# Kernel optimization log

Measured on AMD Instinct MI355X. Metric: run time of the kernel, lower is better.

The kernel has to match this reference:

```python
import jax, jax.numpy as jnp
import numpy as np

B, D, H, W, K = 32, 64, 64, 64, 512  # batch, embed_dim (channels), latent HxW, codebook size
BETA = 0.2


def setup_inputs() -> dict:
    key = jax.random.key(0)
    k1, k2 = jax.random.split(key)
    features = jax.random.normal(k1, (B, D, H, W), dtype=jnp.float32)
    emb_weight = jax.random.normal(k2, (K, D), dtype=jnp.float32)
    return {"features": features, "emb_weight": emb_weight}


def reference(features, emb_weight):
    b, d, h, w = features.shape
    # NCHW -> (B, HW, D) channels-last flatten (torch permute(0,2,3,1).view)
    quant_in = features.transpose(0, 2, 3, 1).reshape(b, h * w, d)
    # squared euclidean distances (argmin-equivalent to torch.cdist)
    x2 = jnp.sum(quant_in * quant_in, axis=-1, keepdims=True)          # (B, HW, 1)
    e2 = jnp.sum(emb_weight * emb_weight, axis=-1)                     # (K,)
    dist2 = x2 + e2[None, None, :] - 2.0 * jnp.einsum('bnd,kd->bnk', quant_in, emb_weight)
    min_index = jnp.argmin(dist2, axis=-1)                             # (B, HW)
    quant_out = emb_weight[min_index]                                  # gather, (B, HW, D)
    # commitment + beta * codebook loss (means over all elements)
    commitment_loss = jnp.mean((jax.lax.stop_gradient(quant_out) - quant_in) ** 2)
    codebook_loss = jnp.mean((quant_out - jax.lax.stop_gradient(quant_in)) ** 2)
    quantize_loss = commitment_loss + BETA * codebook_loss
    # straight-through estimator
    st = quant_in + jax.lax.stop_gradient(quant_out - quant_in)
    st = st.reshape(b, h, w, d).transpose(0, 3, 1, 2)                  # back to NCHW
    return st, quantize_loss
```

## Files before the change

### kernel.cpp

```cpp
#include <hip/hip_runtime.h>
#include <hip/hip_bf16.h>

#define BB 32
#define DD 64
#define HWHW 4096
#define NPOS 131072
#define NELEM (NPOS * DD)
#define KK 512
#define LOSS_SCALE (1.2f / 8388608.f)
#define DELTA 2.0f
#define QCAP 4096
#define PT 2
#define NTHR 1024
#define POSB 512
#define NBLK (NPOS / POSB)

typedef __attribute__((ext_vector_type(8))) short short8v;
typedef __attribute__((ext_vector_type(4))) float float4v;

__device__ inline unsigned short f2bf(float f) {
    unsigned u = __float_as_uint(f);
    unsigned r = u + 0x7FFFu + ((u >> 16) & 1u);
    return (unsigned short)(r >> 16);
}
__device__ inline float bf2f(unsigned short s) {
    return __uint_as_float(((unsigned)s) << 16);
}
__device__ inline unsigned f2o(float f) {
    unsigned u = __float_as_uint(f);
    return ((int)u < 0) ? ~u : (u | 0x80000000u);
}

__global__ __launch_bounds__(256) void vq_prep(const float* __restrict__ emb,
                                               unsigned short* __restrict__ ebf,
                                               float* __restrict__ ne2h) {
    const int t = blockIdx.x * 256 + threadIdx.x;
    const int row = t >> 4, c = t & 15;
    const float4 v = *(const float4*)(emb + row * DD + c * 4);
    unsigned u0 = (unsigned)f2bf(v.x) | ((unsigned)f2bf(v.y) << 16);
    unsigned u1 = (unsigned)f2bf(v.z) | ((unsigned)f2bf(v.w) << 16);
    *(uint2*)(ebf + row * DD + c * 4) = make_uint2(u0, u1);
    float p = v.x * v.x + v.y * v.y + v.z * v.z + v.w * v.w;
    p += __shfl_xor(p, 1, 64); p += __shfl_xor(p, 2, 64);
    p += __shfl_xor(p, 4, 64); p += __shfl_xor(p, 8, 64);
    if (c == 0) ne2h[row] = -0.5f * p;
}

__global__ __launch_bounds__(NTHR) void vq_main(
        const float* __restrict__ feat,
        const float* __restrict__ emb,
        const unsigned short* __restrict__ ebf,
        const float* __restrict__ ne2h,
        float* __restrict__ out,
        float* __restrict__ loss) {

    __shared__ uint4 ebf_lds[4096];
    __shared__ float ne2_lds[KK];
    __shared__ unsigned long long sbest[POSB];
    __shared__ unsigned qbuf[QCAP];
    __shared__ unsigned qcnt;
    __shared__ float wsum[NTHR / 64];

    const int tid = threadIdx.x;
    const int wid = tid >> 6, lane = tid & 63;
    const int l15 = lane & 15, lg = lane >> 4;

    {
        const uint4* src = (const uint4*)ebf;
#pragma unroll
        for (int i = 0; i < 4; ++i) {
            const int idx = tid * 4 + i;
            const int row = idx >> 3, c = idx & 7;
            ebf_lds[row * 8 + (c ^ (row & 7))] = src[idx];
        }
    }
    if (tid < KK) ne2_lds[tid] = ne2h[tid];
    if (tid < POSB) sbest[tid] = 0ull;
    if (tid == 0) qcnt = 0u;

    const int pbase = blockIdx.x * POSB;
    const int b     = pbase >> 12;
    const int hwb   = pbase & 4095;
    const float* featB = feat + (size_t)b * DD * HWHW;
    float*       outB  = out  + (size_t)b * DD * HWHW;
    const int wbase = wid * (PT * 16);

    float xv[PT][2][8];
#pragma unroll
    for (int pt = 0; pt < PT; ++pt) {
        const int hw = hwb + wbase + pt * 16 + l15;
#pragma unroll
        for (int h = 0; h < 2; ++h)
#pragma unroll
            for (int j = 0; j < 8; ++j)
                xv[pt][h][j] = featB[(size_t)(h * 32 + lg * 8 + j) * HWHW + hw];
    }
    short8v bx[PT][2];
#pragma unroll
    for (int pt = 0; pt < PT; ++pt)
#pragma unroll
        for (int h = 0; h < 2; ++h) {
            short8v s;
#pragma unroll
            for (int j = 0; j < 8; ++j) s[j] = (short)f2bf(xv[pt][h][j]);
            bx[pt][h] = s;
        }

    __syncthreads();

    const int swz = l15 & 7;
    const uint4* a0p = &ebf_lds[l15 * 8 + (lg ^ swz)];
    const uint4* a1p = &ebf_lds[l15 * 8 + ((lg | 4) ^ swz)];

    float M[PT];
#pragma unroll
    for (int pt = 0; pt < PT; ++pt) M[pt] = -3.0e38f;

    short8v a0n = *(const short8v*)a0p;
    short8v a1n = *(const short8v*)a1p;
    float4v ne2n = *(const float4v*)&ne2_lds[lg * 4];

    for (int ct = 0; ct < 32; ++ct) {
        const short8v a0c = a0n, a1c = a1n;
        const float4v ne2c = ne2n;
        if (ct < 31) {
            a0n = *(const short8v*)(a0p + (ct + 1) * 128);
            a1n = *(const short8v*)(a1p + (ct + 1) * 128);
            ne2n = *(const float4v*)&ne2_lds[(ct + 1) * 16 + lg * 4];
        }
        float4v acc[PT];
#pragma unroll
        for (int pt = 0; pt < PT; ++pt)
            acc[pt] = __builtin_amdgcn_mfma_f32_16x16x32_bf16(a0c, bx[pt][0], ne2c, 0, 0, 0);
#pragma unroll
        for (int pt = 0; pt < PT; ++pt)
            acc[pt] = __builtin_amdgcn_mfma_f32_16x16x32_bf16(a1c, bx[pt][1], acc[pt], 0, 0, 0);
#pragma unroll
        for (int pt = 0; pt < PT; ++pt) {
            const float m01 = fmaxf(acc[pt][0], acc[pt][1]);
            const float m23 = fmaxf(acc[pt][2], acc[pt][3]);
            M[pt] = fmaxf(M[pt], fmaxf(m01, m23));
        }
    }

    float thr[PT];
#pragma unroll
    for (int pt = 0; pt < PT; ++pt) {
        float m = M[pt];
        m = fmaxf(m, __shfl_xor(m, 16, 64));
        m = fmaxf(m, __shfl_xor(m, 32, 64));
        thr[pt] = m - DELTA;
    }

    a0n = *(const short8v*)a0p;
    a1n = *(const short8v*)a1p;
    ne2n = *(const float4v*)&ne2_lds[lg * 4];

    for (int ct = 0; ct < 32; ++ct) {
        const short8v a0c = a0n, a1c = a1n;
        const float4v ne2c = ne2n;
        if (ct < 31) {
            a0n = *(const short8v*)(a0p + (ct + 1) * 128);
            a1n = *(const short8v*)(a1p + (ct + 1) * 128);
            ne2n = *(const float4v*)&ne2_lds[(ct + 1) * 16 + lg * 4];
        }
        float4v acc[PT];
#pragma unroll
        for (int pt = 0; pt < PT; ++pt)
            acc[pt] = __builtin_amdgcn_mfma_f32_16x16x32_bf16(a0c, bx[pt][0], ne2c, 0, 0, 0);
#pragma unroll
        for (int pt = 0; pt < PT; ++pt)
            acc[pt] = __builtin_amdgcn_mfma_f32_16x16x32_bf16(a1c, bx[pt][1], acc[pt], 0, 0, 0);
#pragma unroll
        for (int pt = 0; pt < PT; ++pt) {
            const float m01 = fmaxf(acc[pt][0], acc[pt][1]);
            const float m23 = fmaxf(acc[pt][2], acc[pt][3]);
            const float mx  = fmaxf(m01, m23);
            if (__any(mx >= thr[pt])) {
#pragma unroll
                for (int r = 0; r < 4; ++r) {
                    if (acc[pt][r] >= thr[pt]) {
                        const unsigned idx  = atomicAdd(&qcnt, 1u);
                        const unsigned code = (unsigned)(ct * 16 + lg * 4 + r);
                        const unsigned pos  = (unsigned)(wbase + pt * 16 + l15);
                        if (idx < QCAP) qbuf[idx] = (pos << 9) | code;
                    }
                }
            }
        }
    }

    __syncthreads();

    const unsigned qn  = qcnt;
    const bool     ovf = (qn > (unsigned)QCAP);
    const unsigned n   = ovf ? (unsigned)(POSB * KK) : qn;
    for (unsigned i = tid; i < n; i += NTHR) {
        unsigned p, k;
        if (ovf) { p = i >> 9; k = i & 511u; }
        else     { const unsigned e = qbuf[i]; p = e >> 9; k = e & 511u; }
        const float4* er4 = (const float4*)(emb + k * DD);
        const float*  fp  = featB + hwb + p;
        float a0 = 0.f, a1 = 0.f;
#pragma unroll 4
        for (int dq = 0; dq < 16; ++dq) {
            const float4 e4 = er4[dq];
            a0 = fmaf(fp[(size_t)(4 * dq    ) * HWHW], e4.x, a0);
            a1 = fmaf(fp[(size_t)(4 * dq + 1) * HWHW], e4.y, a1);
            a0 = fmaf(fp[(size_t)(4 * dq + 2) * HWHW], e4.z, a0);
            a1 = fmaf(fp[(size_t)(4 * dq + 3) * HWHW], e4.w, a1);
        }
        const float sc = (a0 + a1) + ne2h[k];
        const unsigned long long key =
            ((unsigned long long)f2o(sc) << 32) | (unsigned long long)(511u - k);
        atomicMax(&sbest[p], key);
    }

    __syncthreads();

    float lsum = 0.f;
#pragma unroll
    for (int pt = 0; pt < PT; ++pt) {
        const int pl = wbase + pt * 16 + l15;
        const int hw = hwb + pl;
        const unsigned long long key = sbest[pl];
        const unsigned k = 511u - (unsigned)key;
        const float* er = emb + k * DD;
#pragma unroll
        for (int h = 0; h < 2; ++h) {
            const short8v xs = bx[pt][h];
#pragma unroll
            for (int jj = 0; jj < 2; ++jj) {
                const float4v ev = *(const float4v*)(er + h * 32 + lg * 8 + jj * 4);
#pragma unroll
                for (int c = 0; c < 4; ++c) {
                    const int j = jj * 4 + c;
                    const int d = h * 32 + lg * 8 + j;
                    const float q = ev[c];
                    outB[(size_t)d * HWHW + hw] = q;
                    const float diff = q - bf2f((unsigned short)xs[j]);
                    lsum = fmaf(diff, diff, lsum);
                }
            }
        }
    }

#pragma unroll
    for (int off = 32; off > 0; off >>= 1) lsum += __shfl_down(lsum, off, 64);
    if (lane == 0) wsum[wid] = lsum;
    __syncthreads();
    if (tid == 0) {
        float s = 0.f;
#pragma unroll
        for (int w = 0; w < NTHR / 64; ++w) s += wsum[w];
        atomicAdd(loss, s * LOSS_SCALE);
    }
}

extern "C" void kernel_launch(void* const* d_in, const int* in_sizes, int n_in,
                              void* d_out, int out_size, void* d_ws, size_t ws_size,
                              hipStream_t stream) {
    const float* feat = (const float*)d_in[0];
    const float* emb  = (const float*)d_in[1];
    float* out  = (float*)d_out;
    float* loss = out + NELEM;

    unsigned short* ebf  = (unsigned short*)d_ws;
    float*          ne2h = (float*)((char*)d_ws + 64 * 1024);

    hipMemsetAsync(loss, 0, sizeof(float), stream);
    vq_prep<<<dim3(32), dim3(256), 0, stream>>>(emb, ebf, ne2h);
    vq_main<<<dim3(NBLK), dim3(NTHR), 0, stream>>>(feat, emb, ebf, ne2h, out, loss);
}
```

Before: 135.0 us.

## Fuse max pass and candidate collection into single pass with running threshold

```diff
diff --git a/kernel.cpp b/kernel.cpp
--- a/kernel.cpp
+++ b/kernel.cpp
@@ -112,7 +112,7 @@
     const uint4* a0p = &ebf_lds[l15 * 8 + (lg ^ swz)];
     const uint4* a1p = &ebf_lds[l15 * 8 + ((lg | 4) ^ swz)];
 
-    float M[PT];
+    float M[PT], thr[PT];
 #pragma unroll
     for (int pt = 0; pt < PT; ++pt) M[pt] = -3.0e38f;
 
@@ -120,14 +120,12 @@
     short8v a1n = *(const short8v*)a1p;
     float4v ne2n = *(const float4v*)&ne2_lds[lg * 4];
 
-    for (int ct = 0; ct < 32; ++ct) {
+    for (int ct = 0; ct < 4; ++ct) {
         const short8v a0c = a0n, a1c = a1n;
         const float4v ne2c = ne2n;
-        if (ct < 31) {
-            a0n = *(const short8v*)(a0p + (ct + 1) * 128);
-            a1n = *(const short8v*)(a1p + (ct + 1) * 128);
-            ne2n = *(const float4v*)&ne2_lds[(ct + 1) * 16 + lg * 4];
-        }
+        a0n = *(const short8v*)(a0p + (ct + 1) * 128);
+        a1n = *(const short8v*)(a1p + (ct + 1) * 128);
+        ne2n = *(const float4v*)&ne2_lds[(ct + 1) * 16 + lg * 4];
         float4v acc[PT];
 #pragma unroll
         for (int pt = 0; pt < PT; ++pt)
@@ -137,33 +135,22 @@
             acc[pt] = __builtin_amdgcn_mfma_f32_16x16x32_bf16(a1c, bx[pt][1], acc[pt], 0, 0, 0);
 #pragma unroll
         for (int pt = 0; pt < PT; ++pt) {
-            const float m01 = fmaxf(acc[pt][0], acc[pt][1]);
-            const float m23 = fmaxf(acc[pt][2], acc[pt][3]);
-            M[pt] = fmaxf(M[pt], fmaxf(m01, m23));
-        }
-    }
-
-    float thr[PT];
+            const float m4 = fmaxf(fmaxf(fmaxf(acc[pt][0], acc[pt][1]), acc[pt][2]), acc[pt][3]);
+            M[pt] = fmaxf(M[pt], m4);
+        }
+    }
 #pragma unroll
     for (int pt = 0; pt < PT; ++pt) {
         float m = M[pt];
         m = fmaxf(m, __shfl_xor(m, 16, 64));
         m = fmaxf(m, __shfl_xor(m, 32, 64));
-        thr[pt] = m - DELTA;
-    }
-
-    a0n = *(const short8v*)a0p;
-    a1n = *(const short8v*)a1p;
-    ne2n = *(const float4v*)&ne2_lds[lg * 4];
-
-    for (int ct = 0; ct < 32; ++ct) {
-        const short8v a0c = a0n, a1c = a1n;
-        const float4v ne2c = ne2n;
-        if (ct < 31) {
-            a0n = *(const short8v*)(a0p + (ct + 1) * 128);
-            a1n = *(const short8v*)(a1p + (ct + 1) * 128);
-            ne2n = *(const float4v*)&ne2_lds[(ct + 1) * 16 + lg * 4];
-        }
+        M[pt] = m; thr[pt] = m - DELTA;
+    }
+
+    for (int ct = 0; ct < 4; ++ct) {
+        const short8v a0c = *(const short8v*)(a0p + ct * 128);
+        const short8v a1c = *(const short8v*)(a1p + ct * 128);
+        const float4v ne2c = *(const float4v*)&ne2_lds[ct * 16 + lg * 4];
         float4v acc[PT];
 #pragma unroll
         for (int pt = 0; pt < PT; ++pt)
@@ -173,10 +160,8 @@
             acc[pt] = __builtin_amdgcn_mfma_f32_16x16x32_bf16(a1c, bx[pt][1], acc[pt], 0, 0, 0);
 #pragma unroll
         for (int pt = 0; pt < PT; ++pt) {
-            const float m01 = fmaxf(acc[pt][0], acc[pt][1]);
-            const float m23 = fmaxf(acc[pt][2], acc[pt][3]);
-            const float mx  = fmaxf(m01, m23);
-            if (__any(mx >= thr[pt])) {
+            const float m4 = fmaxf(fmaxf(fmaxf(acc[pt][0], acc[pt][1]), acc[pt][2]), acc[pt][3]);
+            if (__any(m4 >= thr[pt])) {
 #pragma unroll
                 for (int r = 0; r < 4; ++r) {
                     if (acc[pt][r] >= thr[pt]) {
@@ -186,6 +171,48 @@
                         if (idx < QCAP) qbuf[idx] = (pos << 9) | code;
                     }
                 }
+            }
+        }
+    }
+
+    for (int ct = 4; ct < 32; ++ct) {
+        const short8v a0c = a0n, a1c = a1n;
+        const float4v ne2c = ne2n;
+        if (ct < 31) {
+            a0n = *(const short8v*)(a0p + (ct + 1) * 128);
+            a1n = *(const short8v*)(a1p + (ct + 1) * 128);
+            ne2n = *(const float4v*)&ne2_lds[(ct + 1) * 16 + lg * 4];
+        }
+        float4v acc[PT];
+#pragma unroll
+        for (int pt = 0; pt < PT; ++pt)
+            acc[pt] = __builtin_amdgcn_mfma_f32_16x16x32_bf16(a0c, bx[pt][0], ne2c, 0, 0, 0);
+#pragma unroll
+        for (int pt = 0; pt < PT; ++pt)
+            acc[pt] = __builtin_amdgcn_mfma_f32_16x16x32_bf16(a1c, bx[pt][1], acc[pt], 0, 0, 0);
+#pragma unroll
+        for (int pt = 0; pt < PT; ++pt) {
+            const float m4 = fmaxf(fmaxf(fmaxf(acc[pt][0], acc[pt][1]), acc[pt][2]), acc[pt][3]);
+            M[pt] = fmaxf(M[pt], m4);
+            if (__any(m4 >= thr[pt])) {
+#pragma unroll
+                for (int r = 0; r < 4; ++r) {
+                    if (acc[pt][r] >= thr[pt]) {
+                        const unsigned idx  = atomicAdd(&qcnt, 1u);
+                        const unsigned code = (unsigned)(ct * 16 + lg * 4 + r);
+                        const unsigned pos  = (unsigned)(wbase + pt * 16 + l15);
+                        if (idx < QCAP) qbuf[idx] = (pos << 9) | code;
+                    }
+                }
+            }
+        }
+        if ((ct & 3) == 3) {
+#pragma unroll
+            for (int pt = 0; pt < PT; ++pt) {
+                float m = M[pt];
+                m = fmaxf(m, __shfl_xor(m, 16, 64));
+                m = fmaxf(m, __shfl_xor(m, 32, 64));
+                M[pt] = m; thr[pt] = m - DELTA;
             }
         }
     }
```

After: 178.9 us. 32.4% more time.

## Split codebook across two wave halves, each wave handling four position tiles

Applied to the files above, without the earlier changes.

```diff
diff --git a/kernel.cpp b/kernel.cpp
--- a/kernel.cpp
+++ b/kernel.cpp
@@ -10,7 +10,7 @@
 #define LOSS_SCALE (1.2f / 8388608.f)
 #define DELTA 2.0f
 #define QCAP 4096
-#define PT 2
+#define PT 4
 #define NTHR 1024
 #define POSB 512
 #define NBLK (NPOS / POSB)
@@ -56,6 +56,7 @@
 
     __shared__ uint4 ebf_lds[4096];
     __shared__ float ne2_lds[KK];
+    __shared__ float pmax2[2][POSB];
     __shared__ unsigned long long sbest[POSB];
     __shared__ unsigned qbuf[QCAP];
     __shared__ unsigned qcnt;
@@ -64,6 +65,8 @@
     const int tid = threadIdx.x;
     const int wid = tid >> 6, lane = tid & 63;
     const int l15 = lane & 15, lg = lane >> 4;
+    const int half = wid >> 3;
+    const int wg   = wid & 7;
 
     {
         const uint4* src = (const uint4*)ebf;
@@ -83,34 +86,38 @@
     const int hwb   = pbase & 4095;
     const float* featB = feat + (size_t)b * DD * HWHW;
     float*       outB  = out  + (size_t)b * DD * HWHW;
-    const int wbase = wid * (PT * 16);
-
-    float xv[PT][2][8];
-#pragma unroll
-    for (int pt = 0; pt < PT; ++pt) {
-        const int hw = hwb + wbase + pt * 16 + l15;
-#pragma unroll
-        for (int h = 0; h < 2; ++h)
-#pragma unroll
-            for (int j = 0; j < 8; ++j)
-                xv[pt][h][j] = featB[(size_t)(h * 32 + lg * 8 + j) * HWHW + hw];
-    }
+    const int wbase = wg * (PT * 16);
+    const int kbase = half * 256;
+
     short8v bx[PT][2];
 #pragma unroll
-    for (int pt = 0; pt < PT; ++pt)
-#pragma unroll
-        for (int h = 0; h < 2; ++h) {
-            short8v s;
-#pragma unroll
-            for (int j = 0; j < 8; ++j) s[j] = (short)f2bf(xv[pt][h][j]);
-            bx[pt][h] = s;
-        }
+    for (int pp = 0; pp < 2; ++pp) {
+        float xv[2][2][8];
+#pragma unroll
+        for (int q = 0; q < 2; ++q) {
+            const int hw = hwb + wbase + (pp * 2 + q) * 16 + l15;
+#pragma unroll
+            for (int h = 0; h < 2; ++h)
+#pragma unroll
+                for (int j = 0; j < 8; ++j)
+                    xv[q][h][j] = featB[(size_t)(h * 32 + lg * 8 + j) * HWHW + hw];
+        }
+#pragma unroll
+        for (int q = 0; q < 2; ++q)
+#pragma unroll
+            for (int h = 0; h < 2; ++h) {
+                short8v s;
+#pragma unroll
+                for (int j = 0; j < 8; ++j) s[j] = (short)f2bf(xv[q][h][j]);
+                bx[pp * 2 + q][h] = s;
+            }
+    }
 
     __syncthreads();
 
     const int swz = l15 & 7;
-    const uint4* a0p = &ebf_lds[l15 * 8 + (lg ^ swz)];
-    const uint4* a1p = &ebf_lds[l15 * 8 + ((lg | 4) ^ swz)];
+    const uint4* a0p = &ebf_lds[(kbase + l15) * 8 + (lg ^ swz)];
+    const uint4* a1p = &ebf_lds[(kbase + l15) * 8 + ((lg | 4) ^ swz)];
 
     float M[PT];
 #pragma unroll
@@ -118,15 +125,15 @@
 
     short8v a0n = *(const short8v*)a0p;
     short8v a1n = *(const short8v*)a1p;
-    float4v ne2n = *(const float4v*)&ne2_lds[lg * 4];
-
-    for (int ct = 0; ct < 32; ++ct) {
+    float4v ne2n = *(const float4v*)&ne2_lds[kbase + lg * 4];
+
+    for (int ct = 0; ct < 16; ++ct) {
         const short8v a0c = a0n, a1c = a1n;
         const float4v ne2c = ne2n;
-        if (ct < 31) {
+        if (ct < 15) {
             a0n = *(const short8v*)(a0p + (ct + 1) * 128);
             a1n = *(const short8v*)(a1p + (ct + 1) * 128);
-            ne2n = *(const float4v*)&ne2_lds[(ct + 1) * 16 + lg * 4];
+            ne2n = *(const float4v*)&ne2_lds[kbase + (ct + 1) * 16 + lg * 4];
         }
         float4v acc[PT];
 #pragma unroll
@@ -143,26 +150,33 @@
         }
     }
 
-    float thr[PT];
 #pragma unroll
     for (int pt = 0; pt < PT; ++pt) {
         float m = M[pt];
         m = fmaxf(m, __shfl_xor(m, 16, 64));
         m = fmaxf(m, __shfl_xor(m, 32, 64));
-        thr[pt] = m - DELTA;
+        if (lg == 0) pmax2[half][wbase + pt * 16 + l15] = m;
+    }
+    __syncthreads();
+
+    float thr[PT];
+#pragma unroll
+    for (int pt = 0; pt < PT; ++pt) {
+        const int pos = wbase + pt * 16 + l15;
+        thr[pt] = fmaxf(pmax2[0][pos], pmax2[1][pos]) - DELTA;
     }
 
     a0n = *(const short8v*)a0p;
     a1n = *(const short8v*)a1p;
-    ne2n = *(const float4v*)&ne2_lds[lg * 4];
-
-    for (int ct = 0; ct < 32; ++ct) {
+    ne2n = *(const float4v*)&ne2_lds[kbase + lg * 4];
+
+    for (int ct = 0; ct < 16; ++ct) {
         const short8v a0c = a0n, a1c = a1n;
         const float4v ne2c = ne2n;
-        if (ct < 31) {
+        if (ct < 15) {
             a0n = *(const short8v*)(a0p + (ct + 1) * 128);
             a1n = *(const short8v*)(a1p + (ct + 1) * 128);
-            ne2n = *(const float4v*)&ne2_lds[(ct + 1) * 16 + lg * 4];
+            ne2n = *(const float4v*)&ne2_lds[kbase + (ct + 1) * 16 + lg * 4];
         }
         float4v acc[PT];
 #pragma unroll
@@ -181,7 +195,7 @@
                 for (int r = 0; r < 4; ++r) {
                     if (acc[pt][r] >= thr[pt]) {
                         const unsigned idx  = atomicAdd(&qcnt, 1u);
-                        const unsigned code = (unsigned)(ct * 16 + lg * 4 + r);
+                        const unsigned code = (unsigned)(kbase + ct * 16 + lg * 4 + r);
                         const unsigned pos  = (unsigned)(wbase + pt * 16 + l15);
                         if (idx < QCAP) qbuf[idx] = (pos << 9) | code;
                     }
@@ -210,7 +224,7 @@
             a0 = fmaf(fp[(size_t)(4 * dq + 2) * HWHW], e4.z, a0);
             a1 = fmaf(fp[(size_t)(4 * dq + 3) * HWHW], e4.w, a1);
         }
-        const float sc = (a0 + a1) + ne2h[k];
+        const float sc = (a0 + a1) + ne2_lds[k];
         const unsigned long long key =
             ((unsigned long long)f2o(sc) << 32) | (unsigned long long)(511u - k);
         atomicMax(&sbest[p], key);
@@ -220,7 +234,8 @@
 
     float lsum = 0.f;
 #pragma unroll
-    for (int pt = 0; pt < PT; ++pt) {
+    for (int q = 0; q < 2; ++q) {
+        const int pt = half * 2 + q;
         const int pl = wbase + pt * 16 + l15;
         const int hw = hwb + pl;
         const unsigned long long key = sbest[pl];
@@ -236,9 +251,9 @@
                 for (int c = 0; c < 4; ++c) {
                     const int j = jj * 4 + c;
                     const int d = h * 32 + lg * 8 + j;
-                    const float q = ev[c];
-                    outB[(size_t)d * HWHW + hw] = q;
-                    const float diff = q - bf2f((unsigned short)xs[j]);
+                    const float q2 = ev[c];
+                    outB[(size_t)d * HWHW + hw] = q2;
+                    const float diff = q2 - bf2f((unsigned short)xs[j]);
                     lsum = fmaf(diff, diff, lsum);
                 }
             }
```

Result: slower. 274.3 us (+103.1%).

## Cache per-tile maxima in fp16 registers to skip second-pass MFMA tiles

Applied to the files above, without the earlier changes.

```diff
diff --git a/kernel.cpp b/kernel.cpp
--- a/kernel.cpp
+++ b/kernel.cpp
@@ -1,5 +1,6 @@
 #include <hip/hip_runtime.h>
 #include <hip/hip_bf16.h>
+#include <hip/hip_fp16.h>
 
 #define BB 32
 #define DD 64
@@ -9,6 +10,7 @@
 #define KK 512
 #define LOSS_SCALE (1.2f / 8388608.f)
 #define DELTA 2.0f
+#define MARG 0.0625f
 #define QCAP 4096
 #define PT 2
 #define NTHR 1024
@@ -29,6 +31,11 @@
 __device__ inline unsigned f2o(float f) {
     unsigned u = __float_as_uint(f);
     return ((int)u < 0) ? ~u : (u | 0x80000000u);
+}
+__device__ inline unsigned packh2(float a, float b) {
+    unsigned lo = (unsigned)__half_as_ushort(__float2half(a));
+    unsigned hi = (unsigned)__half_as_ushort(__float2half(b));
+    return lo | (hi << 16);
 }
 
 __global__ __launch_bounds__(256) void vq_prep(const float* __restrict__ emb,
@@ -112,78 +119,78 @@
     const uint4* a0p = &ebf_lds[l15 * 8 + (lg ^ swz)];
     const uint4* a1p = &ebf_lds[l15 * 8 + ((lg | 4) ^ swz)];
 
-    float M[PT];
-#pragma unroll
-    for (int pt = 0; pt < PT; ++pt) M[pt] = -3.0e38f;
-
-    short8v a0n = *(const short8v*)a0p;
-    short8v a1n = *(const short8v*)a1p;
-    float4v ne2n = *(const float4v*)&ne2_lds[lg * 4];
-
+    float M0 = -3.0e38f, M1 = -3.0e38f;
+    unsigned cache_u[32];
+
+#pragma unroll
     for (int ct = 0; ct < 32; ++ct) {
-        const short8v a0c = a0n, a1c = a1n;
-        const float4v ne2c = ne2n;
-        if (ct < 31) {
-            a0n = *(const short8v*)(a0p + (ct + 1) * 128);
-            a1n = *(const short8v*)(a1p + (ct + 1) * 128);
-            ne2n = *(const float4v*)&ne2_lds[(ct + 1) * 16 + lg * 4];
-        }
-        float4v acc[PT];
-#pragma unroll
-        for (int pt = 0; pt < PT; ++pt)
-            acc[pt] = __builtin_amdgcn_mfma_f32_16x16x32_bf16(a0c, bx[pt][0], ne2c, 0, 0, 0);
-#pragma unroll
-        for (int pt = 0; pt < PT; ++pt)
-            acc[pt] = __builtin_amdgcn_mfma_f32_16x16x32_bf16(a1c, bx[pt][1], acc[pt], 0, 0, 0);
-#pragma unroll
-        for (int pt = 0; pt < PT; ++pt) {
-            const float m01 = fmaxf(acc[pt][0], acc[pt][1]);
-            const float m23 = fmaxf(acc[pt][2], acc[pt][3]);
-            M[pt] = fmaxf(M[pt], fmaxf(m01, m23));
-        }
+        const short8v a0c = *(const short8v*)(a0p + ct * 128);
+        const short8v a1c = *(const short8v*)(a1p + ct * 128);
+        const float4v ne2c = *(const float4v*)&ne2_lds[ct * 16 + lg * 4];
+        float4v acc0 = __builtin_amdgcn_mfma_f32_16x16x32_bf16(a0c, bx[0][0], ne2c, 0, 0, 0);
+        acc0 = __builtin_amdgcn_mfma_f32_16x16x32_bf16(a1c, bx[0][1], acc0, 0, 0, 0);
+        float4v acc1 = __builtin_amdgcn_mfma_f32_16x16x32_bf16(a0c, bx[1][0], ne2c, 0, 0, 0);
+        acc1 = __builtin_amdgcn_mfma_f32_16x16x32_bf16(a1c, bx[1][1], acc1, 0, 0, 0);
+        const float m4a = fmaxf(fmaxf(acc0[0], acc0[1]), fmaxf(acc0[2], acc0[3]));
+        const float m4b = fmaxf(fmaxf(acc1[0], acc1[1]), fmaxf(acc1[2], acc1[3]));
+        M0 = fmaxf(M0, m4a);
+        M1 = fmaxf(M1, m4b);
+        cache_u[ct] = packh2(m4a, m4b);
     }
 
     float thr[PT];
-#pragma unroll
-    for (int pt = 0; pt < PT; ++pt) {
-        float m = M[pt];
+    {
+        float m = M0;
         m = fmaxf(m, __shfl_xor(m, 16, 64));
         m = fmaxf(m, __shfl_xor(m, 32, 64));
-        thr[pt] = m - DELTA;
-    }
-
-    a0n = *(const short8v*)a0p;
-    a1n = *(const short8v*)a1p;
-    ne2n = *(const float4v*)&ne2_lds[lg * 4];
-
+        thr[0] = m - DELTA;
+        m = M1;
+        m = fmaxf(m, __shfl_xor(m, 16, 64));
+        m = fmaxf(m, __shfl_xor(m, 32, 64));
+        thr[1] = m - DELTA;
+    }
+    const float tt0 = thr[0] - MARG, tt1 = thr[1] - MARG;
+
+#pragma unroll
     for (int ct = 0; ct < 32; ++ct) {
-        const short8v a0c = a0n, a1c = a1n;
-        const float4v ne2c = ne2n;
-        if (ct < 31) {
-            a0n = *(const short8v*)(a0p + (ct + 1) * 128);
-            a1n = *(const short8v*)(a1p + (ct + 1) * 128);
-            ne2n = *(const float4v*)&ne2_lds[(ct + 1) * 16 + lg * 4];
-        }
-        float4v acc[PT];
-#pragma unroll
-        for (int pt = 0; pt < PT; ++pt)
-            acc[pt] = __builtin_amdgcn_mfma_f32_16x16x32_bf16(a0c, bx[pt][0], ne2c, 0, 0, 0);
-#pragma unroll
-        for (int pt = 0; pt < PT; ++pt)
-            acc[pt] = __builtin_amdgcn_mfma_f32_16x16x32_bf16(a1c, bx[pt][1], acc[pt], 0, 0, 0);
-#pragma unroll
-        for (int pt = 0; pt < PT; ++pt) {
-            const float m01 = fmaxf(acc[pt][0], acc[pt][1]);
-            const float m23 = fmaxf(acc[pt][2], acc[pt][3]);
-            const float mx  = fmaxf(m01, m23);
-            if (__any(mx >= thr[pt])) {
-#pragma unroll
-                for (int r = 0; r < 4; ++r) {
-                    if (acc[pt][r] >= thr[pt]) {
-                        const unsigned idx  = atomicAdd(&qcnt, 1u);
-                        const unsigned code = (unsigned)(ct * 16 + lg * 4 + r);
-                        const unsigned pos  = (unsigned)(wbase + pt * 16 + l15);
-                        if (idx < QCAP) qbuf[idx] = (pos << 9) | code;
+        const unsigned cw = cache_u[ct];
+        const float c0 = __half2float(__ushort_as_half((unsigned short)(cw & 0xffffu)));
+        const float c1 = __half2float(__ushort_as_half((unsigned short)(cw >> 16)));
+        const bool t0 = __any(c0 >= tt0);
+        const bool t1 = __any(c1 >= tt1);
+        if (t0 | t1) {
+            const short8v a0c = *(const short8v*)(a0p + ct * 128);
+            const short8v a1c = *(const short8v*)(a1p + ct * 128);
+            const float4v ne2c = *(const float4v*)&ne2_lds[ct * 16 + lg * 4];
+            if (t0) {
+                float4v acc = __builtin_amdgcn_mfma_f32_16x16x32_bf16(a0c, bx[0][0], ne2c, 0, 0, 0);
+                acc = __builtin_amdgcn_mfma_f32_16x16x32_bf16(a1c, bx[0][1], acc, 0, 0, 0);
+                const float mx = fmaxf(fmaxf(acc[0], acc[1]), fmaxf(acc[2], acc[3]));
+                if (mx >= thr[0]) {
+#pragma unroll
+                    for (int r = 0; r < 4; ++r) {
+                        if (acc[r] >= thr[0]) {
+                            const unsigned idx  = atomicAdd(&qcnt, 1u);
+                            const unsigned code = (unsigned)(ct * 16 + lg * 4 + r);
+                            const unsigned pos  = (unsigned)(wbase + l15);
+                            if (idx < QCAP) qbuf[idx] = (pos << 9) | code;
+                        }
+                    }
+                }
+            }
+            if (t1) {
+                float4v acc = __builtin_amdgcn_mfma_f32_16x16x32_bf16(a0c, bx[1][0], ne2c, 0, 0, 0);
+                acc = __builtin_amdgcn_mfma_f32_16x16x32_bf16(a1c, bx[1][1], acc, 0, 0, 0);
+                const float mx = fmaxf(fmaxf(acc[0], acc[1]), fmaxf(acc[2], acc[3]));
+                if (mx >= thr[1]) {
+#pragma unroll
+                    for (int r = 0; r < 4; ++r) {
+                        if (acc[r] >= thr[1]) {
+                            const unsigned idx  = atomicAdd(&qcnt, 1u);
+                            const unsigned code = (unsigned)(ct * 16 + lg * 4 + r);
+                            const unsigned pos  = (unsigned)(wbase + 16 + l15);
+                            if (idx < QCAP) qbuf[idx] = (pos << 9) | code;
+                        }
                     }
                 }
             }
@@ -210,7 +217,7 @@
             a0 = fmaf(fp[(size_t)(4 * dq + 2) * HWHW], e4.z, a0);
             a1 = fmaf(fp[(size_t)(4 * dq + 3) * HWHW], e4.w, a1);
         }
-        const float sc = (a0 + a1) + ne2h[k];
+        const float sc = (a0 + a1) + ne2_lds[k];
         const unsigned long long key =
             ((unsigned long long)f2o(sc) << 32) | (unsigned long long)(511u - k);
         atomicMax(&sbest[p], key);
```

Measured after the change: 148.8 us. 10.2% more time.
